# Performance work log

Measured on AMD Instinct MI355X. Metric: run time of the kernel, lower is better.

## Reference

```python
import jax, jax.numpy as jnp
import numpy as np

EPS = 1e-5
NEIGHBOR_K = 3
NEG_SLOPE = 0.2

def _conv(x, w):
    # x: [N,C,H,W], w: [O,I,3,3], stride 1, SAME padding
    return jax.lax.conv_general_dilated(
        x, w, window_strides=(1, 1), padding='SAME',
        dimension_numbers=('NCHW', 'OIHW', 'NCHW'))

def _bn(x, gamma, beta):
    # BatchNorm2d in training mode: batch statistics over (N,H,W), biased var
    m = x.mean(axis=(0, 2, 3), keepdims=True)
    v = x.var(axis=(0, 2, 3), keepdims=True)
    xn = (x - m) * jax.lax.rsqrt(v + EPS)
    return xn * gamma.reshape(1, -1, 1, 1) + beta.reshape(1, -1, 1, 1)

def _lrelu(x):
    return jnp.where(x >= 0, x, NEG_SLOPE * x)

def _maxpool2(x):
    return jax.lax.reduce_window(x, -jnp.inf, jax.lax.max,
                                 (1, 1, 2, 2), (1, 1, 2, 2), 'VALID')

def _features(x, w1, g1, b1, w2, g2, b2, w3, g3, b3, w4, g4, b4):
    x = _maxpool2(_lrelu(_bn(_conv(x, w1), g1, b1)))
    x = _maxpool2(_lrelu(_bn(_conv(x, w2), g2, b2)))
    x = _lrelu(_bn(_conv(x, w3), g3, b3))
    x = _lrelu(_bn(_conv(x, w4), g4, b4))
    return x  # [N, 64, 21, 21]

def setup_inputs() -> dict:
    key = jax.random.key(0)
    ks = jax.random.split(key, 8)
    inp = {
        'input1': jax.random.normal(ks[0], (32, 3, 84, 84), jnp.float32),
        'input2': jax.random.normal(ks[1], (5, 5, 3, 84, 84), jnp.float32),
        'w1': jax.random.normal(ks[2], (64, 3, 3, 3), jnp.float32) * 0.1,
        'g1': jax.random.uniform(ks[3], (64,), jnp.float32, 0.5, 1.5),
        'b1': jnp.zeros((64,), jnp.float32),
        'w2': jax.random.normal(ks[4], (64, 64, 3, 3), jnp.float32) * 0.1,
        'g2': jax.random.uniform(ks[5], (64,), jnp.float32, 0.5, 1.5),
        'b2': jnp.zeros((64,), jnp.float32),
        'w3': jax.random.normal(ks[6], (64, 64, 3, 3), jnp.float32) * 0.1,
        'g3': jax.random.uniform(ks[7], (64,), jnp.float32, 0.5, 1.5),
        'b3': jnp.zeros((64,), jnp.float32),
        'w4': jax.random.normal(jax.random.fold_in(key, 100), (64, 64, 3, 3), jnp.float32) * 0.1,
        'g4': jax.random.uniform(jax.random.fold_in(key, 101), (64,), jnp.float32, 0.5, 1.5),
        'b4': jnp.zeros((64,), jnp.float32),
    }
    return inp

def reference(input1, input2, w1, g1, b1, w2, g2, b2, w3, g3, b3, w4, g4, b4):
    params = (w1, g1, b1, w2, g2, b2, w3, g3, b3, w4, g4, b4)
    # Query features: [B, C, h, w]
    q = _features(input1, *params)
    B, C, h, w = q.shape
    hw = h * w
    Q = q.reshape(B, C, hw).transpose(0, 2, 1)            # [B, hw, C]
    qn = jnp.linalg.norm(Q, axis=2, keepdims=True)        # [B, hw, 1]
    # Support features, BN stats per class-batch (matches per-class forward)
    s = jax.vmap(lambda x: _features(x, *params))(input2) # [nc, shot, C, h, w]
    nc, shot = s.shape[0], s.shape[1]
    S = s.transpose(0, 2, 1, 3, 4).reshape(nc, C, shot * hw)  # [nc, C, M]
    sn = jnp.linalg.norm(S, axis=1, keepdims=True)            # [nc, 1, M]
    # Cosine similarities: [B, nc, hw, M]
    sims = jnp.einsum('bqc,ncm->bnqm', Q, S)
    sims = sims / (qn[:, None, :, :] * sn[None, :, :, :])
    topv = jax.lax.top_k(sims, NEIGHBOR_K)[0]              # [B, nc, hw, k]
    return topv.sum(axis=(2, 3))                           # [B, nc]
```

## Files before the change

### kernel.cpp

```cpp
#include <hip/hip_runtime.h>
#include <hip/hip_bf16.h>
#include <stdint.h>

#define NQ 32
#define NCLS 5
#define SHOT 5
#define NIMG 57
#define P1 7056
#define P2 1764
#define P3 441
#define PX 3528
#define MM (SHOT*P3)
#define EPSB 1e-5f
#define SLOPE 0.2f
#define NEGINF -3.4e38f
#define NREP 32
#define MSPAN 576
#define MRNG 4
#define QBLK 128
#define NQB 4
#define QG 2
#define SLS 72

typedef __attribute__((ext_vector_type(8))) short short8;
typedef __attribute__((ext_vector_type(4))) float f32x4;

__device__ __forceinline__ unsigned short bf16bits(float v)
{
    __hip_bfloat16 h = __float2bfloat16(v);
    return *reinterpret_cast<unsigned short*>(&h);
}
__device__ __forceinline__ float bits2f(unsigned short u)
{
    unsigned int x = ((unsigned int)u) << 16;
    return *reinterpret_cast<float*>(&x);
}

__global__ void pack_all_k(const float* __restrict__ w1, const float* __restrict__ w2,
                           const float* __restrict__ w3, const float* __restrict__ w4,
                           unsigned short* __restrict__ wpk1, unsigned short* __restrict__ wpk2,
                           unsigned short* __restrict__ wpk3, unsigned short* __restrict__ wpk4,
                           float* __restrict__ sums)
{
    int i = blockIdx.x * 256 + threadIdx.x;
    if (i < 4 * 6 * 64 * 2 * NREP) sums[i] = 0.f;
    if (i < 3 * 36864) {
        int set = i / 36864, ii = i - set * 36864;
        const float* w = (set == 0) ? w2 : (set == 1) ? w3 : w4;
        unsigned short* wpk = (set == 0) ? wpk2 : (set == 1) ? wpk3 : wpk4;
        int j = ii & 7, lane = (ii >> 3) & 63, chunk = ii >> 9;
        int nt = chunk & 3, half = (chunk >> 2) & 1, t = chunk >> 3;
        int co = nt * 16 + (lane & 15);
        int ci = half * 32 + (lane >> 4) * 8 + j;
        wpk[ii] = bf16bits(w[co * 576 + ci * 9 + t]);
    } else {
        int ii = i - 3 * 36864;
        if (ii >= 4096) return;
        int j = ii & 7, lane = (ii >> 3) & 63, c8 = ii >> 9;
        int nt = c8 & 3, f = c8 >> 2;
        int co = nt * 16 + (lane & 15), q = lane >> 4;
        int k = q * 8 + j;
        float val = 0.f;
        if (f == 0) {
            int t = k >> 2, ci = k & 3;
            if (ci < 3) val = w1[co * 27 + ci * 9 + t];
        } else if (k < 4) {
            int ci = k & 3;
            if (ci < 3) val = w1[co * 27 + ci * 9 + 8];
        }
        wpk1[ii] = bf16bits(val);
    }
}

__global__ __launch_bounds__(256) void conv1m_k(const float* __restrict__ in1,
                                                const float* __restrict__ in2,
                                                const unsigned short* __restrict__ wpk1,
                                                __hip_bfloat16* __restrict__ xpool,
                                                float* __restrict__ sums)
{
    constexpr int S = 84, P = P1, MBLK = 256, NB = 28, SPAN = MBLK + 2 * S + 2;
    __shared__ __align__(16) unsigned short ls4[SPAN * 4];
    __shared__ float qs[4][64], qs2[4][64];
    int img = blockIdx.x / NB;
    int p0 = (blockIdx.x % NB) * MBLK;
    int tid = threadIdx.x, lane = tid & 63, wv = tid >> 6;
    int col = lane & 15, quad = lane >> 4;
    const float* in = (img < NQ) ? in1 + (size_t)img * 3 * P1
                                 : in2 + (size_t)(img - NQ) * 3 * P1;
    for (int u = tid; u < SPAN; u += 256) {
        int p = p0 - S - 1 + u;
        union { unsigned short us[4]; uint2 u2; } o;
        o.u2 = (uint2){0u, 0u};
        if (p >= 0 && p < P) {
            o.us[0] = bf16bits(in[p]);
            o.us[1] = bf16bits(in[P1 + p]);
            o.us[2] = bf16bits(in[2 * P1 + p]);
        }
        *(uint2*)(ls4 + u * 4) = o.u2;
    }
    const short8* wb = (const short8*)wpk1;
    short8 b0[4], b1[4];
    #pragma unroll
    for (int nt = 0; nt < 4; ++nt) {
        b0[nt] = wb[(size_t)(nt * 64 + lane)];
        b1[nt] = wb[(size_t)((4 + nt) * 64 + lane)];
    }
    int t0 = 2 * quad, t1 = t0 + 1;
    int d0 = (t0 / 3 - 1) * S + (t0 % 3 - 1);
    int d1 = (t1 / 3 - 1) * S + (t1 % 3 - 1);
    const int d8 = S + 1;
    int tx0 = t0 % 3, tx1 = t1 % 3;
    __syncthreads();
    f32x4 acc[4][4];
    #pragma unroll
    for (int mt = 0; mt < 4; ++mt)
        #pragma unroll
        for (int nt = 0; nt < 4; ++nt) acc[mt][nt] = (f32x4){0.f, 0.f, 0.f, 0.f};
    #pragma unroll
    for (int mt = 0; mt < 4; ++mt) {
        int pl = wv * 64 + mt * 16 + col;
        int xm = (p0 + pl) % S;
        int base = pl + S + 1;
        uint2 h0 = *(const uint2*)(ls4 + (base + d0) * 4);
        uint2 h1 = *(const uint2*)(ls4 + (base + d1) * 4);
        uint2 h8 = *(const uint2*)(ls4 + (base + d8) * 4);
        bool ok0 = (tx0 == 0) ? (xm >= 1) : ((tx0 == 2) ? (xm <= S - 2) : true);
        bool ok1 = (tx1 == 0) ? (xm >= 1) : ((tx1 == 2) ? (xm <= S - 2) : true);
        bool ok8 = (quad == 0) && (xm <= S - 2);
        if (!ok0) h0 = (uint2){0u, 0u};
        if (!ok1) h1 = (uint2){0u, 0u};
        if (!ok8) h8 = (uint2){0u, 0u};
        union { uint4 u; short8 s; } ca, cb;
        ca.u = (uint4){h0.x, h0.y, h1.x, h1.y};
        cb.u = (uint4){h8.x, h8.y, 0u, 0u};
        #pragma unroll
        for (int nt = 0; nt < 4; ++nt) {
            acc[mt][nt] = __builtin_amdgcn_mfma_f32_16x16x32_bf16(ca.s, b0[nt], acc[mt][nt], 0, 0, 0);
            acc[mt][nt] = __builtin_amdgcn_mfma_f32_16x16x32_bf16(cb.s, b1[nt], acc[mt][nt], 0, 0, 0);
        }
    }
    float s[4] = {0.f, 0.f, 0.f, 0.f}, s2[4] = {0.f, 0.f, 0.f, 0.f};
    __hip_bfloat16* ob = xpool + (size_t)img * PX * 64;
    #pragma unroll
    for (int mt = 0; mt < 4; ++mt) {
        int tb = p0 + wv * 64 + mt * 16 + quad * 4;
        #pragma unroll
        for (int reg = 0; reg < 4; ++reg) {
            int pr = tb + reg;
            if (pr < P) {
                #pragma unroll
                for (int nt = 0; nt < 4; ++nt) {
                    float v = acc[mt][nt][reg];
                    s[nt] += v;
                    s2[nt] = fmaf(v, v, s2[nt]);
                }
            }
        }
        #pragma unroll
        for (int pr2 = 0; pr2 < 2; ++pr2) {
            int m0 = tb + pr2 * 2;
            if (m0 < P) {
                #pragma unroll
                for (int nt = 0; nt < 4; ++nt) {
                    float v = fmaxf(acc[mt][nt][pr2 * 2], acc[mt][nt][pr2 * 2 + 1]);
                    ob[(size_t)(m0 >> 1) * 64 + nt * 16 + col] = __float2bfloat16(v);
                }
            }
        }
    }
    #pragma unroll
    for (int d = 16; d < 64; d <<= 1)
        #pragma unroll
        for (int nt = 0; nt < 4; ++nt) {
            s[nt] += __shfl_xor(s[nt], d, 64);
            s2[nt] += __shfl_xor(s2[nt], d, 64);
        }
    if (quad == 0) {
        #pragma unroll
        for (int nt = 0; nt < 4; ++nt) {
            qs[wv][nt * 16 + col] = s[nt];
            qs2[wv][nt * 16 + col] = s2[nt];
        }
    }
    __syncthreads();
    if (wv == 0) {
        int g = (img < NQ) ? 0 : 1 + (img - NQ) / SHOT;
        int rep = blockIdx.x & (NREP - 1);
        float ts = qs[0][lane] + qs[1][lane] + qs[2][lane] + qs[3][lane];
        float ts2 = qs2[0][lane] + qs2[1][lane] + qs2[2][lane] + qs2[3][lane];
        float* base = sums + ((size_t)(g * 64 + lane) * 2) * NREP + rep;
        atomicAdd(base, ts);
        atomicAdd(base + NREP, ts2);
    }
}

template <int S, int MBLK, int MODE, bool POOLX>
__global__ __launch_bounds__(256) void conv64m_k(const unsigned short* __restrict__ inv,
                                                 const unsigned short* __restrict__ wpk,
                                                 __hip_bfloat16* __restrict__ out,
                                                 float* __restrict__ sums,
                                                 const float* __restrict__ msin)
{
    constexpr int P = S * S;
    constexpr int MT = MBLK / 64;
    constexpr int NB = (P + MBLK - 1) / MBLK;
    constexpr int SPAN = MBLK + 2 * S + 2;
    __shared__ __align__(16) unsigned short ls[SPAN * 72];
    __shared__ float qs[4][64], qs2[4][64];
    int img = blockIdx.x / NB;
    int p0 = (blockIdx.x % NB) * MBLK;
    int tid = threadIdx.x;
    int lane = tid & 63, wv = tid >> 6;
    int col = lane & 15, quad = lane >> 4;
    int g = (img < NQ) ? 0 : 1 + (img - NQ) / SHOT;
    if constexpr (MODE == 0) {
        const unsigned short* ib = inv + (size_t)img * P * 64;
        for (int u = tid; u < SPAN * 8; u += 256) {
            int pix = u >> 3, part = u & 7;
            int p = p0 - S - 1 + pix;
            short8 v = {0, 0, 0, 0, 0, 0, 0, 0};
            if (p >= 0 && p < P) v = *(const short8*)(ib + (size_t)p * 64 + part * 8);
            *(short8*)(ls + pix * 72 + part * 8) = v;
        }
    } else {
        int part = tid & 7;
        float ba[8], bb[8];
        #pragma unroll
        for (int j = 0; j < 8; ++j) {
            float2 ab = ((const float2*)msin)[g * 64 + part * 8 + j];
            ba[j] = ab.x;
            bb[j] = ab.y;
        }
        if constexpr (MODE == 1) {
            const unsigned short* ib = inv + (size_t)img * P * 64;
            for (int u = tid; u < SPAN * 8; u += 256) {
                int pix = u >> 3;
                int p = p0 - S - 1 + pix;
                union { unsigned short us[8]; short8 s8; } o;
                #pragma unroll
                for (int j = 0; j < 8; ++j) o.us[j] = 0;
                if (p >= 0 && p < P) {
                    union { short8 s8; unsigned short us[8]; } x;
                    x.s8 = *(const short8*)(ib + (size_t)p * 64 + part * 8);
                    #pragma unroll
                    for (int j = 0; j < 8; ++j) {
                        float v = fmaf(bits2f(x.us[j]), ba[j], bb[j]);
                        v = fmaxf(v, SLOPE * v);
                        o.us[j] = bf16bits(v);
                    }
                }
                *(short8*)(ls + pix * 72 + part * 8) = o.s8;
            }
        } else {
            const unsigned short* ib2 = inv + (size_t)img * (2 * (size_t)P) * 64;
            for (int u = tid; u < SPAN * 8; u += 256) {
                int pix = u >> 3;
                int p = p0 - S - 1 + pix;
                union { unsigned short us[8]; short8 s8; } o;
                #pragma unroll
                for (int j = 0; j < 8; ++j) o.us[j] = 0;
                if (p >= 0 && p < P) {
                    int y = p / S, x = p - y * S;
                    const unsigned short* src = ib2 + ((size_t)(2 * y) * S + x) * 64 + part * 8;
                    union { short8 s8; unsigned short us[8]; } x0, x1;
                    x0.s8 = *(const short8*)src;
                    x1.s8 = *(const short8*)(src + (size_t)S * 64);
                    #pragma unroll
                    for (int j = 0; j < 8; ++j) {
                        float v = fmaxf(bits2f(x0.us[j]), bits2f(x1.us[j]));
                        v = fmaf(v, ba[j], bb[j]);
                        v = fmaxf(v, SLOPE * v);
                        o.us[j] = bf16bits(v);
                    }
                }
                *(short8*)(ls + pix * 72 + part * 8) = o.s8;
            }
        }
    }
    __syncthreads();
    f32x4 acc[MT][4];
    #pragma unroll
    for (int mt = 0; mt < MT; ++mt)
        #pragma unroll
        for (int nt = 0; nt < 4; ++nt) acc[mt][nt] = (f32x4){0.f, 0.f, 0.f, 0.f};
    bool mok0[MT], mok2[MT];
    #pragma unroll
    for (int mt = 0; mt < MT; ++mt) {
        int xm = (p0 + wv * (MT * 16) + mt * 16 + col) % S;
        mok0[mt] = xm >= 1;
        mok2[mt] = xm <= S - 2;
    }
    const short8* wb = (const short8*)wpk;
    #pragma unroll
    for (int ky = 0; ky < 3; ++ky) {
        #pragma unroll
        for (int kx = 0; kx < 3; ++kx) {
            int t = ky * 3 + kx;
            int d = (ky - 1) * S + (kx - 1);
            #pragma unroll
            for (int half = 0; half < 2; ++half) {
                short8 b[4];
                #pragma unroll
                for (int nt = 0; nt < 4; ++nt)
                    b[nt] = wb[((t * 2 + half) * 4 + nt) * 64 + lane];
                #pragma unroll
                for (int mt = 0; mt < MT; ++mt) {
                    int idx = wv * (MT * 16) + mt * 16 + col + S + 1 + d;
                    short8 a = *(const short8*)(ls + idx * 72 + half * 32 + quad * 8);
                    bool ok = (kx == 0) ? mok0[mt] : (kx == 2) ? mok2[mt] : true;
                    if (!ok) a = (short8){0, 0, 0, 0, 0, 0, 0, 0};
                    #pragma unroll
                    for (int nt = 0; nt < 4; ++nt)
                        acc[mt][nt] = __builtin_amdgcn_mfma_f32_16x16x32_bf16(a, b[nt], acc[mt][nt], 0, 0, 0);
                }
            }
        }
    }
    float s[4] = {0.f, 0.f, 0.f, 0.f}, s2[4] = {0.f, 0.f, 0.f, 0.f};
    __hip_bfloat16* ob = out + (size_t)img * (POOLX ? P / 2 : P) * 64;
    #pragma unroll
    for (int mt = 0; mt < MT; ++mt) {
        int tb = p0 + wv * (MT * 16) + mt * 16 + quad * 4;
        #pragma unroll
        for (int reg = 0; reg < 4; ++reg) {
            int pr = tb + reg;
            if (pr < P) {
                #pragma unroll
                for (int nt = 0; nt < 4; ++nt) {
                    float v = acc[mt][nt][reg];
                    s[nt] += v;
                    s2[nt] = fmaf(v, v, s2[nt]);
                }
            }
        }
        if constexpr (POOLX) {
            #pragma unroll
            for (int pr2 = 0; pr2 < 2; ++pr2) {
                int m0 = tb + pr2 * 2;
                if (m0 < P) {
                    #pragma unroll
                    for (int nt = 0; nt < 4; ++nt) {
                        float v = fmaxf(acc[mt][nt][pr2 * 2], acc[mt][nt][pr2 * 2 + 1]);
                        ob[(size_t)(m0 >> 1) * 64 + nt * 16 + col] = __float2bfloat16(v);
                    }
                }
            }
        } else {
            #pragma unroll
            for (int reg = 0; reg < 4; ++reg) {
                int pr = tb + reg;
                if (pr < P) {
                    #pragma unroll
                    for (int nt = 0; nt < 4; ++nt)
                        ob[(size_t)pr * 64 + nt * 16 + col] = __float2bfloat16(acc[mt][nt][reg]);
                }
            }
        }
    }
    #pragma unroll
    for (int d = 16; d < 64; d <<= 1)
        #pragma unroll
        for (int nt = 0; nt < 4; ++nt) {
            s[nt] += __shfl_xor(s[nt], d, 64);
            s2[nt] += __shfl_xor(s2[nt], d, 64);
        }
    if (quad == 0) {
        #pragma unroll
        for (int nt = 0; nt < 4; ++nt) {
            qs[wv][nt * 16 + col] = s[nt];
            qs2[wv][nt * 16 + col] = s2[nt];
        }
    }
    __syncthreads();
    if (wv == 0) {
        int rep = blockIdx.x & (NREP - 1);
        float ts = qs[0][lane] + qs[1][lane] + qs[2][lane] + qs[3][lane];
        float ts2 = qs2[0][lane] + qs2[1][lane] + qs2[2][lane] + qs2[3][lane];
        float* base = sums + ((size_t)(g * 64 + lane) * 2) * NREP + rep;
        atomicAdd(base, ts);
        atomicAdd(base + NREP, ts2);
    }
}

__global__ void finalize_k(const float* __restrict__ sums, float* __restrict__ ms,
                           const float* __restrict__ gamma, const float* __restrict__ beta, int P)
{
    int i = blockIdx.x * blockDim.x + threadIdx.x;
    if (i >= 6 * 64) return;
    int g = i >> 6, c = i & 63;
    const float* ps = sums + (size_t)i * 2 * NREP;
    float s = 0.f, s2 = 0.f;
    #pragma unroll
    for (int r = 0; r < NREP; ++r) { s += ps[r]; s2 += ps[NREP + r]; }
    float cnt = (float)((g == 0 ? NQ : SHOT) * P);
    float mean = s / cnt;
    float var = s2 / cnt - mean * mean;
    float a = rsqrtf(var + EPSB) * gamma[c];
    ms[i * 2] = a;
    ms[i * 2 + 1] = fmaf(-mean, a, beta[c]);
}

__global__ __launch_bounds__(256) void bnnorm_k(const unsigned short* __restrict__ x,
                                                const float* __restrict__ ms,
                                                __hip_bfloat16* __restrict__ out)
{
    int lane = threadIdx.x & 63, wvr = threadIdx.x >> 6;
    int pix = blockIdx.x * 4 + wvr;
    if (pix >= NIMG * P3) return;
    int img = pix / P3;
    int g = (img < NQ) ? 0 : 1 + (img - NQ) / SHOT;
    float v = fmaf(bits2f(x[(size_t)pix * 64 + lane]), ms[(g * 64 + lane) * 2], ms[(g * 64 + lane) * 2 + 1]);
    v = v >= 0.f ? v : SLOPE * v;
    float ss = v * v;
    #pragma unroll
    for (int d = 32; d > 0; d >>= 1) ss += __shfl_xor(ss, d, 64);
    out[(size_t)pix * 64 + lane] = __float2bfloat16(v * rsqrtf(ss));
}

__device__ __forceinline__ void ins3(float v, float& t0, float& t1, float& t2)
{
    t2 = __builtin_amdgcn_fmed3f(v, t1, t2);
    t1 = __builtin_amdgcn_fmed3f(v, t0, t1);
    t0 = fmaxf(t0, v);
}

template <int PAT>
__device__ __forceinline__ void swzmerge(float& t0, float& t1, float& t2)
{
    float u0 = __int_as_float(__builtin_amdgcn_ds_swizzle(__float_as_int(t0), PAT));
    float u1 = __int_as_float(__builtin_amdgcn_ds_swizzle(__float_as_int(t1), PAT));
    float u2 = __int_as_float(__builtin_amdgcn_ds_swizzle(__float_as_int(t2), PAT));
    ins3(u0, t0, t1, t2);
    ins3(u1, t0, t1, t2);
    ins3(u2, t0, t1, t2);
}

__global__ __launch_bounds__(256) void sim_part_k(const __hip_bfloat16* __restrict__ fhat,
                                                  float* __restrict__ part)
{
    __shared__ __align__(16) unsigned short sl[2][64 * SLS];
    int t = blockIdx.x;
    int mr = t & 3;
    int qb = (t >> 2) & 3;
    int n = (t >> 4) % NCLS;
    int bq = t / (16 * NCLS);
    int tid = threadIdx.x, lane = tid & 63, wv = tid >> 6;
    int col = lane & 15, quad = lane >> 4;
    short8 a0[QG], a1[QG];
    #pragma unroll
    for (int g = 0; g < QG; ++g) {
        int q = qb * QBLK + wv * (QG * 16) + g * 16 + col;
        int qc = q < P3 ? q : P3 - 1;
        const unsigned short* qp = (const unsigned short*)fhat + ((size_t)bq * P3 + qc) * 64;
        a0[g] = *(const short8*)(qp + quad * 8);
        a1[g] = *(const short8*)(qp + 32 + quad * 8);
    }
    const unsigned short* sp = (const unsigned short*)fhat + (size_t)(NQ + n * SHOT) * P3 * 64;
    int m_lo = mr * MSPAN;
    int m_cnt = MM - m_lo; if (m_cnt > MSPAN) m_cnt = MSPAN;
    int nfull = m_cnt >> 6;
    int rem = m_cnt & 63;
    float t0[QG][4], t1[QG][4], t2[QG][4];
    #pragma unroll
    for (int g = 0; g < QG; ++g)
        #pragma unroll
        for (int r = 0; r < 4; ++r) { t0[g][r] = NEGINF; t1[g][r] = NEGINF; t2[g][r] = NEGINF; }
    int srow = tid >> 3, scc = (tid & 7) * 8;
    const unsigned short* gp = sp + (size_t)(m_lo + srow) * 64 + scc;
    unsigned short* ld0 = &sl[0][srow * SLS + scc];
    unsigned short* ld1 = &sl[1][srow * SLS + scc];
    const short8 z8 = {0, 0, 0, 0, 0, 0, 0, 0};
    short8 v0 = *(const short8*)gp;
    short8 v1 = *(const short8*)(gp + 32 * 64);
    *(short8*)ld0 = v0;
    *(short8*)(ld0 + 32 * SLS) = v1;
    __syncthreads();
    int cur = 0;
    for (int c = 0; c < nfull; ++c) {
        bool nf = (c + 1 < nfull);
        bool np = (c + 1 == nfull) && (rem != 0);
        if (nf) {
            gp += 64 * 64;
            v0 = *(const short8*)gp;
            v1 = *(const short8*)(gp + 32 * 64);
        } else if (np) {
            gp += 64 * 64;
            v0 = (srow < rem) ? *(const short8*)gp : z8;
            v1 = z8;
        }
        const unsigned short* sr = &sl[cur][col * SLS + quad * 8];
        #pragma unroll
        for (int mt = 0; mt < 4; ++mt) {
            short8 b0 = *(const short8*)(sr + mt * (16 * SLS));
            short8 b1 = *(const short8*)(sr + mt * (16 * SLS) + 32);
            #pragma unroll
            for (int g = 0; g < QG; ++g) {
                f32x4 acc = {0.f, 0.f, 0.f, 0.f};
                acc = __builtin_amdgcn_mfma_f32_16x16x32_bf16(a0[g], b0, acc, 0, 0, 0);
                acc = __builtin_amdgcn_mfma_f32_16x16x32_bf16(a1[g], b1, acc, 0, 0, 0);
                #pragma unroll
                for (int r = 0; r < 4; ++r) ins3(acc[r], t0[g][r], t1[g][r], t2[g][r]);
            }
        }
        if (nf | np) {
            unsigned short* ld = (cur == 0) ? ld1 : ld0;
            *(short8*)ld = v0;
            *(short8*)(ld + 32 * SLS) = v1;
        }
        __syncthreads();
        cur ^= 1;
    }
    if (rem) {
        const unsigned short* sr = &sl[cur][col * SLS + quad * 8];
        int ptiles = (rem + 15) >> 4;
        for (int mt = 0; mt < ptiles; ++mt) {
            short8 b0 = *(const short8*)(sr + mt * (16 * SLS));
            short8 b1 = *(const short8*)(sr + mt * (16 * SLS) + 32);
            bool valid = (mt * 16 + col) < rem;
            #pragma unroll
            for (int g = 0; g < QG; ++g) {
                f32x4 acc = {0.f, 0.f, 0.f, 0.f};
                acc = __builtin_amdgcn_mfma_f32_16x16x32_bf16(a0[g], b0, acc, 0, 0, 0);
                acc = __builtin_amdgcn_mfma_f32_16x16x32_bf16(a1[g], b1, acc, 0, 0, 0);
                #pragma unroll
                for (int r = 0; r < 4; ++r)
                    ins3(valid ? acc[r] : NEGINF, t0[g][r], t1[g][r], t2[g][r]);
            }
        }
    }
    #pragma unroll
    for (int g = 0; g < QG; ++g)
        #pragma unroll
        for (int r = 0; r < 4; ++r) {
            swzmerge<0x041F>(t0[g][r], t1[g][r], t2[g][r]);
            swzmerge<0x081F>(t0[g][r], t1[g][r], t2[g][r]);
            swzmerge<0x101F>(t0[g][r], t1[g][r], t2[g][r]);
            swzmerge<0x201F>(t0[g][r], t1[g][r], t2[g][r]);
        }
    if (col == 0) {
        #pragma unroll
        for (int g = 0; g < QG; ++g)
            #pragma unroll
            for (int r = 0; r < 4; ++r) {
                int ql = wv * (QG * 16) + g * 16 + quad * 4 + r;
                float* pp = part + ((((size_t)(bq * NCLS + n) * NQB + qb) * MRNG + mr) * QBLK + ql) * 3;
                pp[0] = t0[g][r];
                pp[1] = t1[g][r];
                pp[2] = t2[g][r];
            }
    }
}

__global__ __launch_bounds__(256) void sim_merge_k(const float* __restrict__ part,
                                                   float* __restrict__ out)
{
    __shared__ float red[4];
    int b = blockIdx.x;
    int tid = threadIdx.x, lane = tid & 63, wv = tid >> 6;
    float s = 0.f;
    for (int q = tid; q < P3; q += 256) {
        int qb = q >> 7, ql = q & 127;
        const float* pp = part + (((size_t)b * NQB + qb) * MRNG * QBLK + ql) * 3;
        float v0 = pp[0], v1 = pp[1], v2 = pp[2];
        #pragma unroll
        for (int mr = 1; mr < 4; ++mr) {
            const float* pm = pp + (size_t)mr * (QBLK * 3);
            ins3(pm[0], v0, v1, v2);
            ins3(pm[1], v0, v1, v2);
            ins3(pm[2], v0, v1, v2);
        }
        s += v0 + v1 + v2;
    }
    #pragma unroll
    for (int d = 32; d > 0; d >>= 1) s += __shfl_xor(s, d, 64);
    if (lane == 0) red[wv] = s;
    __syncthreads();
    if (tid == 0) out[b] = red[0] + red[1] + red[2] + red[3];
}

extern "C" void kernel_launch(void* const* d_in, const int* in_sizes, int n_in,
                              void* d_out, int out_size, void* d_ws, size_t ws_size,
                              hipStream_t stream)
{
    const float* input1 = (const float*)d_in[0];
    const float* input2 = (const float*)d_in[1];
    const float* w1 = (const float*)d_in[2];
    const float* g1 = (const float*)d_in[3];
    const float* b1 = (const float*)d_in[4];
    const float* w2 = (const float*)d_in[5];
    const float* g2 = (const float*)d_in[6];
    const float* b2 = (const float*)d_in[7];
    const float* w3 = (const float*)d_in[8];
    const float* g3 = (const float*)d_in[9];
    const float* b3 = (const float*)d_in[10];
    const float* w4 = (const float*)d_in[11];
    const float* g4 = (const float*)d_in[12];
    const float* b4 = (const float*)d_in[13];
    float* out = (float*)d_out;

    char* w8 = (char*)d_ws;
    const size_t oB = 51480576;
    const size_t oT = oB + 12870144;
    const size_t STG = 6 * 64 * 2 * NREP * sizeof(float);
    __hip_bfloat16* xpool1 = (__hip_bfloat16*)(w8 + 0);
    __hip_bfloat16* conv3raw = (__hip_bfloat16*)(w8 + 0);
    __hip_bfloat16* conv4raw = (__hip_bfloat16*)(w8 + 9652608);
    __hip_bfloat16* fhat = (__hip_bfloat16*)(w8 + 16087680);
    __hip_bfloat16* xpool2 = (__hip_bfloat16*)(w8 + oB);
    float* sums = (float*)(w8 + oT);
    float* ms = (float*)(w8 + oT + 4 * STG);
    unsigned short* wpk2 = (unsigned short*)(w8 + oT + 4 * STG + 12288);
    unsigned short* wpk3 = (unsigned short*)(w8 + oT + 4 * STG + 12288 + 73728);
    unsigned short* wpk4 = (unsigned short*)(w8 + oT + 4 * STG + 12288 + 147456);
    unsigned short* wpk1 = (unsigned short*)(w8 + oT + 4 * STG + 12288 + 221184);
    const size_t oP = oT + 4 * STG + 12288 + 221184 + 8192;
    float* part = (float*)(w8 + oP);
    if (ws_size < oP + (size_t)NQ * NCLS * NQB * MRNG * QBLK * 3 * sizeof(float)) return;
    float* sums1 = sums;
    float* sums2 = sums + 6 * 64 * 2 * NREP;
    float* sums3 = sums2 + 6 * 64 * 2 * NREP;
    float* sums4 = sums3 + 6 * 64 * 2 * NREP;

    pack_all_k<<<448, 256, 0, stream>>>(w1, w2, w3, w4, wpk1, wpk2, wpk3, wpk4, sums);

    conv1m_k<<<NIMG * 28, 256, 0, stream>>>(input1, input2, wpk1, xpool1, sums1);
    finalize_k<<<2, 256, 0, stream>>>(sums1, ms + 0, g1, b1, P1);
    conv64m_k<42, 256, 2, true><<<NIMG * 7, 256, 0, stream>>>(
        (const unsigned short*)xpool1, wpk2, xpool2, sums2, ms + 0);
    finalize_k<<<2, 256, 0, stream>>>(sums2, ms + 768, g2, b2, P2);
    conv64m_k<21, 128, 2, false><<<NIMG * 4, 256, 0, stream>>>(
        (const unsigned short*)xpool2, wpk3, conv3raw, sums3, ms + 768);
    finalize_k<<<2, 256, 0, stream>>>(sums3, ms + 1536, g3, b3, P3);
    conv64m_k<21, 128, 1, false><<<NIMG * 4, 256, 0, stream>>>(
        (const unsigned short*)conv3raw, wpk4, conv4raw, sums4, ms + 1536);
    finalize_k<<<2, 256, 0, stream>>>(sums4, ms + 2304, g4, b4, P3);
    bnnorm_k<<<6285, 256, 0, stream>>>((const unsigned short*)conv4raw, ms + 2304, fhat);
    sim_part_k<<<NQ * NCLS * NQB * MRNG, 256, 0, stream>>>(fhat, part);
    sim_merge_k<<<NQ * NCLS, 256, 0, stream>>>(part, out);
}
```

Before: 223.2 us.

## Fold BN finalize into consumer kernels and halve similarity M-range split

Removes the four small finalize_k launches by having each consumer block (the conv64m kernels and bnnorm_k) reduce the previous layer's replicated sums into per-block shared-memory scale/shift. This cuts kernel launch and serialization overhead between stages, at the cost of every block redundantly re-reading 64 channels × 64 partial sums. It also halves the M-range split in the similarity kernel (MRNG 4→2, MSPAN doubled), so there are fewer blocks each doing more work and less partial top-k data to merge. The dead MODE 0 path is dropped.

```diff
diff --git a/kernel.cpp b/kernel.cpp
--- a/kernel.cpp
+++ b/kernel.cpp
@@ -15,8 +15,8 @@
 #define SLOPE 0.2f
 #define NEGINF -3.4e38f
 #define NREP 32
-#define MSPAN 576
-#define MRNG 4
+#define MSPAN 1152
+#define MRNG 2
 #define QBLK 128
 #define NQB 4
 #define QG 2
@@ -194,12 +194,34 @@
     }
 }
 
-template <int S, int MBLK, int MODE, bool POOLX>
+template <int PREVP>
+__device__ __forceinline__ void bn_fold(const float* __restrict__ sums_prev,
+                                        const float* __restrict__ gamma,
+                                        const float* __restrict__ beta,
+                                        int g, int tid, float* msl)
+{
+    if (tid < 64) {
+        const float* ps = sums_prev + (size_t)(g * 64 + tid) * 2 * NREP;
+        float s = 0.f, s2 = 0.f;
+        #pragma unroll
+        for (int r = 0; r < NREP; ++r) { s += ps[r]; s2 += ps[NREP + r]; }
+        float cnt = (float)((g == 0 ? NQ : SHOT) * PREVP);
+        float mean = s / cnt;
+        float var = s2 / cnt - mean * mean;
+        float a = rsqrtf(var + EPSB) * gamma[tid];
+        msl[tid * 2] = a;
+        msl[tid * 2 + 1] = fmaf(-mean, a, beta[tid]);
+    }
+}
+
+template <int S, int MBLK, int MODE, bool POOLX, int PREVP>
 __global__ __launch_bounds__(256) void conv64m_k(const unsigned short* __restrict__ inv,
                                                  const unsigned short* __restrict__ wpk,
                                                  __hip_bfloat16* __restrict__ out,
                                                  float* __restrict__ sums,
-                                                 const float* __restrict__ msin)
+                                                 const float* __restrict__ sums_prev,
+                                                 const float* __restrict__ gamma,
+                                                 const float* __restrict__ beta)
 {
     constexpr int P = S * S;
     constexpr int MT = MBLK / 64;
@@ -207,29 +229,22 @@
     constexpr int SPAN = MBLK + 2 * S + 2;
     __shared__ __align__(16) unsigned short ls[SPAN * 72];
     __shared__ float qs[4][64], qs2[4][64];
+    __shared__ float msl[128];
     int img = blockIdx.x / NB;
     int p0 = (blockIdx.x % NB) * MBLK;
     int tid = threadIdx.x;
     int lane = tid & 63, wv = tid >> 6;
     int col = lane & 15, quad = lane >> 4;
     int g = (img < NQ) ? 0 : 1 + (img - NQ) / SHOT;
-    if constexpr (MODE == 0) {
-        const unsigned short* ib = inv + (size_t)img * P * 64;
-        for (int u = tid; u < SPAN * 8; u += 256) {
-            int pix = u >> 3, part = u & 7;
-            int p = p0 - S - 1 + pix;
-            short8 v = {0, 0, 0, 0, 0, 0, 0, 0};
-            if (p >= 0 && p < P) v = *(const short8*)(ib + (size_t)p * 64 + part * 8);
-            *(short8*)(ls + pix * 72 + part * 8) = v;
-        }
-    } else {
+    bn_fold<PREVP>(sums_prev, gamma, beta, g, tid, msl);
+    __syncthreads();
+    {
         int part = tid & 7;
         float ba[8], bb[8];
         #pragma unroll
         for (int j = 0; j < 8; ++j) {
-            float2 ab = ((const float2*)msin)[g * 64 + part * 8 + j];
-            ba[j] = ab.x;
-            bb[j] = ab.y;
+            ba[j] = msl[(part * 8 + j) * 2];
+            bb[j] = msl[(part * 8 + j) * 2 + 1];
         }
         if constexpr (MODE == 1) {
             const unsigned short* ib = inv + (size_t)img * P * 64;
@@ -382,34 +397,28 @@
     }
 }
 
-__global__ void finalize_k(const float* __restrict__ sums, float* __restrict__ ms,
-                           const float* __restrict__ gamma, const float* __restrict__ beta, int P)
-{
-    int i = blockIdx.x * blockDim.x + threadIdx.x;
-    if (i >= 6 * 64) return;
-    int g = i >> 6, c = i & 63;
-    const float* ps = sums + (size_t)i * 2 * NREP;
-    float s = 0.f, s2 = 0.f;
-    #pragma unroll
-    for (int r = 0; r < NREP; ++r) { s += ps[r]; s2 += ps[NREP + r]; }
-    float cnt = (float)((g == 0 ? NQ : SHOT) * P);
-    float mean = s / cnt;
-    float var = s2 / cnt - mean * mean;
-    float a = rsqrtf(var + EPSB) * gamma[c];
-    ms[i * 2] = a;
-    ms[i * 2 + 1] = fmaf(-mean, a, beta[c]);
-}
-
 __global__ __launch_bounds__(256) void bnnorm_k(const unsigned short* __restrict__ x,
-                                                const float* __restrict__ ms,
+                                                const float* __restrict__ sums_prev,
+                                                const float* __restrict__ g4,
+                                                const float* __restrict__ b4,
                                                 __hip_bfloat16* __restrict__ out)
 {
-    int lane = threadIdx.x & 63, wvr = threadIdx.x >> 6;
-    int pix = blockIdx.x * 4 + wvr;
+    __shared__ float msl[2][128];
+    int tid = threadIdx.x;
+    int pix0 = blockIdx.x * 4;
+    int img0 = pix0 / P3, img3 = (pix0 + 3) / P3;
+    int ga = (img0 < NQ) ? 0 : 1 + (img0 - NQ) / SHOT;
+    int gb = (img3 < NIMG) ? ((img3 < NQ) ? 0 : 1 + (img3 - NQ) / SHOT) : ga;
+    bn_fold<P3>(sums_prev, g4, b4, ga, tid, msl[0]);
+    if (gb != ga) bn_fold<P3>(sums_prev, g4, b4, gb, tid, msl[1]);
+    __syncthreads();
+    int lane = tid & 63, wvr = tid >> 6;
+    int pix = pix0 + wvr;
     if (pix >= NIMG * P3) return;
     int img = pix / P3;
     int g = (img < NQ) ? 0 : 1 + (img - NQ) / SHOT;
-    float v = fmaf(bits2f(x[(size_t)pix * 64 + lane]), ms[(g * 64 + lane) * 2], ms[(g * 64 + lane) * 2 + 1]);
+    const float* ms = msl[(g == ga) ? 0 : 1];
+    float v = fmaf(bits2f(x[(size_t)pix * 64 + lane]), ms[lane * 2], ms[lane * 2 + 1]);
     v = v >= 0.f ? v : SLOPE * v;
     float ss = v * v;
     #pragma unroll
@@ -440,10 +449,10 @@
 {
     __shared__ __align__(16) unsigned short sl[2][64 * SLS];
     int t = blockIdx.x;
-    int mr = t & 3;
-    int qb = (t >> 2) & 3;
-    int n = (t >> 4) % NCLS;
-    int bq = t / (16 * NCLS);
+    int mr = t & 1;
+    int qb = (t >> 1) & 3;
+    int n = (t >> 3) % NCLS;
+    int bq = t / (8 * NCLS);
     int tid = threadIdx.x, lane = tid & 63, wv = tid >> 6;
     int col = lane & 15, quad = lane >> 4;
     short8 a0[QG], a1[QG];
@@ -563,7 +572,7 @@
         const float* pp = part + (((size_t)b * NQB + qb) * MRNG * QBLK + ql) * 3;
         float v0 = pp[0], v1 = pp[1], v2 = pp[2];
         #pragma unroll
-        for (int mr = 1; mr < 4; ++mr) {
+        for (int mr = 1; mr < MRNG; ++mr) {
             const float* pm = pp + (size_t)mr * (QBLK * 3);
             ins3(pm[0], v0, v1, v2);
             ins3(pm[1], v0, v1, v2);
@@ -608,7 +617,6 @@
     __hip_bfloat16* fhat = (__hip_bfloat16*)(w8 + 16087680);
     __hip_bfloat16* xpool2 = (__hip_bfloat16*)(w8 + oB);
     float* sums = (float*)(w8 + oT);
-    float* ms = (float*)(w8 + oT + 4 * STG);
     unsigned short* wpk2 = (unsigned short*)(w8 + oT + 4 * STG + 12288);
     unsigned short* wpk3 = (unsigned short*)(w8 + oT + 4 * STG + 12288 + 73728);
     unsigned short* wpk4 = (unsigned short*)(w8 + oT + 4 * STG + 12288 + 147456);
@@ -624,17 +632,13 @@
     pack_all_k<<<448, 256, 0, stream>>>(w1, w2, w3, w4, wpk1, wpk2, wpk3, wpk4, sums);
 
     conv1m_k<<<NIMG * 28, 256, 0, stream>>>(input1, input2, wpk1, xpool1, sums1);
-    finalize_k<<<2, 256, 0, stream>>>(sums1, ms + 0, g1, b1, P1);
-    conv64m_k<42, 256, 2, true><<<NIMG * 7, 256, 0, stream>>>(
-        (const unsigned short*)xpool1, wpk2, xpool2, sums2, ms + 0);
-    finalize_k<<<2, 256, 0, stream>>>(sums2, ms + 768, g2, b2, P2);
-    conv64m_k<21, 128, 2, false><<<NIMG * 4, 256, 0, stream>>>(
-        (const unsigned short*)xpool2, wpk3, conv3raw, sums3, ms + 768);
-    finalize_k<<<2, 256, 0, stream>>>(sums3, ms + 1536, g3, b3, P3);
-    conv64m_k<21, 128, 1, false><<<NIMG * 4, 256, 0, stream>>>(
-        (const unsigned short*)conv3raw, wpk4, conv4raw, sums4, ms + 1536);
-    finalize_k<<<2, 256, 0, stream>>>(sums4, ms + 2304, g4, b4, P3);
-    bnnorm_k<<<6285, 256, 0, stream>>>((const unsigned short*)conv4raw, ms + 2304, fhat);
+    conv64m_k<42, 256, 2, true, P1><<<NIMG * 7, 256, 0, stream>>>(
+        (const unsigned short*)xpool1, wpk2, xpool2, sums2, sums1, g1, b1);
+    conv64m_k<21, 128, 2, false, P2><<<NIMG * 4, 256, 0, stream>>>(
+        (const unsigned short*)xpool2, wpk3, conv3raw, sums3, sums2, g2, b2);
+    conv64m_k<21, 128, 1, false, P3><<<NIMG * 4, 256, 0, stream>>>(
+        (const unsigned short*)conv3raw, wpk4, conv4raw, sums4, sums3, g3, b3);
+    bnnorm_k<<<6285, 256, 0, stream>>>((const unsigned short*)conv4raw, sums4, g4, b4, fhat);
     sim_part_k<<<NQ * NCLS * NQB * MRNG, 256, 0, stream>>>(fhat, part);
     sim_merge_k<<<NQ * NCLS, 256, 0, stream>>>(part, out);
 }
```

New measurement: 215.9 us. 3.3% less time.
